# Kernel optimization log

Hardware: AMD Instinct MI355X
Metric: run time of the kernel (lower is better)

Reference implementation:

```python
import jax, jax.numpy as jnp
import numpy as np

EPS_DIST = 1e-8
EPS_BN = 1e-5


def _bn_relu(x, g, b):
    # training-mode BatchNorm1d over (batch, spatial) per channel, then ReLU
    mean = jnp.mean(x, axis=(0, 2), keepdims=True)
    var = jnp.mean((x - mean) ** 2, axis=(0, 2), keepdims=True)
    xhat = (x - mean) * jax.lax.rsqrt(var + EPS_BN)
    return jax.nn.relu(xhat * g[None, :, None] + b[None, :, None])


def setup_inputs() -> dict:
    key = jax.random.key(0)
    ks = jax.random.split(key, 8)
    B, N, M, C1, C2 = 8, 16384, 4096, 64, 256
    return {
        "p1": jax.random.normal(ks[0], (B, N, 3), jnp.float32),
        "p2": jax.random.normal(ks[1], (B, M, 3), jnp.float32),
        "f1": jax.random.normal(ks[2], (B, C1, N), jnp.float32),
        "f2": jax.random.normal(ks[3], (B, C2, M), jnp.float32),
        "idx": jax.random.randint(ks[4], (B, N, 3), 0, M, jnp.int64),
        "W1": jax.random.normal(ks[5], (256, C1 + C2), jnp.float32) * 0.05,
        "g1": jnp.ones((256,), jnp.float32),
        "b1": jnp.zeros((256,), jnp.float32),
        "W2": jax.random.normal(ks[6], (256, 256), jnp.float32) * 0.05,
        "g2": jnp.ones((256,), jnp.float32),
        "b2": jnp.zeros((256,), jnp.float32),
    }


def reference(p1, p2, f1, f2, idx, W1, g1, b1, W2, g2, b2):
    B = p1.shape[0]
    b_ix = jnp.arange(B)[:, None, None]  # batch index for gathers
    # --- three_interpolation: inverse-squared-distance weighted 3-NN interp ---
    nbr_xyz = p2[b_ix, idx]                     # [B, N, 3, 3]
    d2 = jnp.sum((p1[:, :, None, :] - nbr_xyz) ** 2, axis=-1)  # [B, N, 3]
    recip = 1.0 / (d2 + EPS_DIST)
    weight = recip / jnp.sum(recip, axis=-1, keepdims=True)    # [B, N, 3]
    f2_nbr = jnp.swapaxes(f2, 1, 2)[b_ix, idx]  # [B, N, 3, C2]
    interp = jnp.einsum("bnkc,bnk->bcn", f2_nbr, weight)       # [B, C2, N]
    # --- concat + two 1x1 conv + BN + ReLU blocks ---
    x = jnp.concatenate((f1, interp), axis=1)   # [B, C1+C2, N]
    x = _bn_relu(jnp.einsum("oi,bin->bon", W1, x), g1, b1)
    x = _bn_relu(jnp.einsum("oi,bin->bon", W2, x), g2, b2)
    return x
```

## Files before the change

kernel.cpp:

```cpp
#include <hip/hip_runtime.h>
#include <hip/hip_bf16.h>

#define BB 8
#define NN 16384
#define MM 4096
#define C1 64
#define C2 256
#define K1 320
#define CO 256
#define MTOT (BB * NN)

#define STATS_OFF 0
#define FLAG_OFF  8192
#define W1B_OFF   16384
#define W2B_OFF   180224
#define F2T_OFF   327680
#define XT_OFF    (327680 + 16777216)
#define H2_OFF    (327680 + 16777216 + 83886080)

typedef short v8s __attribute__((ext_vector_type(8)));
typedef float v4f __attribute__((ext_vector_type(4)));

__device__ __forceinline__ float bf2f(unsigned short u) {
    unsigned v = ((unsigned)u) << 16;
    float f;
    __builtin_memcpy(&f, &v, 4);
    return f;
}
__device__ __forceinline__ unsigned short f2bf(float f) {
    unsigned u;
    __builtin_memcpy(&u, &f, 4);
    unsigned r = u + 0x7fffu + ((u >> 16) & 1u);
    return (unsigned short)(r >> 16);
}
__device__ __forceinline__ void gload16(const unsigned short* g, unsigned short* l) {
    __builtin_amdgcn_global_load_lds((const __attribute__((address_space(1))) unsigned int*)g,
                                     (__attribute__((address_space(3))) unsigned int*)l, 16, 0, 0);
}

__global__ void k_prep(const void* idx_raw, int* flag64, float* stats,
                       const float* __restrict__ W1, unsigned short* __restrict__ W1b,
                       const float* __restrict__ W2, unsigned short* __restrict__ W2b) {
    int blk = blockIdx.x;
    int t = threadIdx.x;
    if (blk < 320) {
        int e = blk * 256 + t;
        W1b[e] = f2bf(W1[e]);
    } else if (blk < 576) {
        int e = (blk - 320) * 256 + t;
        W2b[e] = f2bf(W2[e]);
    } else {
        for (int i = t; i < 8 * 256; i += 256) stats[i] = 0.f;
        if (t == 0) {
            const int* a = (const int*)idx_raw;
            int all0 = 1;
            for (int j = 1; j < 64; j += 2) all0 &= (a[j] == 0);
            *flag64 = all0;
        }
    }
}

__global__ void k_tr_f2(const float* __restrict__ f2, unsigned short* __restrict__ f2t) {
    __shared__ float tile[64][33];
    int b = blockIdx.z;
    int c0 = blockIdx.y * 64;
    int m0 = blockIdx.x * 32;
    int t = threadIdx.x;
    int lm = t & 31, lc = t >> 5;
    const float* src = f2 + ((size_t)b * C2 + c0) * MM + m0;
#pragma unroll
    for (int j = 0; j < 8; ++j)
        tile[lc + 8 * j][lm] = src[(size_t)(lc + 8 * j) * MM + lm];
    __syncthreads();
    int m = t >> 3, c8 = (t & 7) * 8;
    unsigned short tmp[8];
#pragma unroll
    for (int k = 0; k < 8; ++k) tmp[k] = f2bf(tile[c8 + k][m]);
    uint4 v;
    v.x = (unsigned)tmp[0] | ((unsigned)tmp[1] << 16);
    v.y = (unsigned)tmp[2] | ((unsigned)tmp[3] << 16);
    v.z = (unsigned)tmp[4] | ((unsigned)tmp[5] << 16);
    v.w = (unsigned)tmp[6] | ((unsigned)tmp[7] << 16);
    *(uint4*)&f2t[((size_t)b * MM + m0 + m) * C2 + c0 + c8] = v;
}

__global__ void k_tr_f1(const float* __restrict__ f1, unsigned short* __restrict__ xT) {
    __shared__ float tile[64][33];
    int b = blockIdx.z;
    int n0 = blockIdx.x * 32;
    int t = threadIdx.x;
    int lm = t & 31, lc = t >> 5;
    const float* src = f1 + ((size_t)b * C1) * NN + n0;
#pragma unroll
    for (int j = 0; j < 8; ++j)
        tile[lc + 8 * j][lm] = src[(size_t)(lc + 8 * j) * NN + lm];
    __syncthreads();
    int m = t >> 3, c8 = (t & 7) * 8;
    unsigned short tmp[8];
#pragma unroll
    for (int k = 0; k < 8; ++k) tmp[k] = f2bf(tile[c8 + k][m]);
    uint4 v;
    v.x = (unsigned)tmp[0] | ((unsigned)tmp[1] << 16);
    v.y = (unsigned)tmp[2] | ((unsigned)tmp[3] << 16);
    v.z = (unsigned)tmp[4] | ((unsigned)tmp[5] << 16);
    v.w = (unsigned)tmp[6] | ((unsigned)tmp[7] << 16);
    *(uint4*)&xT[((size_t)b * NN + n0 + m) * K1 + c8] = v;
}

__global__ void k_interp(const float* __restrict__ p1, const float* __restrict__ p2,
                         const void* __restrict__ idxv, const int* __restrict__ flag64,
                         const unsigned short* __restrict__ f2t,
                         unsigned short* __restrict__ xT) {
    int t = threadIdx.x;
    int p = t >> 5, lane = t & 31;
    size_t pt = (size_t)blockIdx.x * 8 + p;
    int b = (int)(pt >> 14);
    int m0, m1, m2;
    if (*flag64) {
        const long long* id = (const long long*)idxv;
        m0 = (int)id[pt * 3 + 0]; m1 = (int)id[pt * 3 + 1]; m2 = (int)id[pt * 3 + 2];
    } else {
        const int* id = (const int*)idxv;
        m0 = id[pt * 3 + 0]; m1 = id[pt * 3 + 1]; m2 = id[pt * 3 + 2];
    }
    float qx = p1[pt * 3 + 0], qy = p1[pt * 3 + 1], qz = p1[pt * 3 + 2];
    const float* pb = p2 + (size_t)b * MM * 3;
    float dx, dy, dz;
    dx = qx - pb[m0 * 3 + 0]; dy = qy - pb[m0 * 3 + 1]; dz = qz - pb[m0 * 3 + 2];
    float d0 = dx * dx + dy * dy + dz * dz;
    dx = qx - pb[m1 * 3 + 0]; dy = qy - pb[m1 * 3 + 1]; dz = qz - pb[m1 * 3 + 2];
    float d1 = dx * dx + dy * dy + dz * dz;
    dx = qx - pb[m2 * 3 + 0]; dy = qy - pb[m2 * 3 + 1]; dz = qz - pb[m2 * 3 + 2];
    float d2v = dx * dx + dy * dy + dz * dz;
    float r0 = 1.f / (d0 + 1e-8f), r1 = 1.f / (d1 + 1e-8f), r2 = 1.f / (d2v + 1e-8f);
    float inv = 1.f / (r0 + r1 + r2);
    float w0 = r0 * inv, w1 = r1 * inv, w2 = r2 * inv;

    const unsigned short* fb = f2t + (size_t)b * MM * C2;
    int c0 = lane * 8;
    uint4 va = *(const uint4*)(fb + (size_t)m0 * C2 + c0);
    uint4 vb = *(const uint4*)(fb + (size_t)m1 * C2 + c0);
    uint4 vc = *(const uint4*)(fb + (size_t)m2 * C2 + c0);

    float r[8];
    {
        const unsigned av[4] = {va.x, va.y, va.z, va.w};
        const unsigned bv[4] = {vb.x, vb.y, vb.z, vb.w};
        const unsigned cv[4] = {vc.x, vc.y, vc.z, vc.w};
#pragma unroll
        for (int q = 0; q < 4; ++q) {
            r[2 * q + 0] = w0 * bf2f((unsigned short)(av[q] & 0xffff))
                         + w1 * bf2f((unsigned short)(bv[q] & 0xffff))
                         + w2 * bf2f((unsigned short)(cv[q] & 0xffff));
            r[2 * q + 1] = w0 * bf2f((unsigned short)(av[q] >> 16))
                         + w1 * bf2f((unsigned short)(bv[q] >> 16))
                         + w2 * bf2f((unsigned short)(cv[q] >> 16));
        }
    }
    uint4 outv;
    outv.x = (unsigned)f2bf(r[0]) | ((unsigned)f2bf(r[1]) << 16);
    outv.y = (unsigned)f2bf(r[2]) | ((unsigned)f2bf(r[3]) << 16);
    outv.z = (unsigned)f2bf(r[4]) | ((unsigned)f2bf(r[5]) << 16);
    outv.w = (unsigned)f2bf(r[6]) | ((unsigned)f2bf(r[7]) << 16);
    *(uint4*)(xT + pt * K1 + C1 + c0) = outv;
}

#define TM 128
#define TN 128
#define TK 64
__launch_bounds__(256)
__global__ void k_gemm1(const unsigned short* __restrict__ xT,
                        const unsigned short* __restrict__ W1b,
                        unsigned short* __restrict__ h1,
                        float* __restrict__ sum1, float* __restrict__ ssq1) {
    __shared__ unsigned short smem[TM * TK + TN * TK];
    __shared__ float s_sum[TN], s_ssq[TN];
    unsigned short* As = smem;
    unsigned short* Bs = smem + TM * TK;
    const int t = threadIdx.x;
    const int lane = t & 63, w = t >> 6;
    const int wm = w >> 1, wc = w & 1;
    const long rbase = (long)blockIdx.x * TM;
    const int cb = blockIdx.y * TN;

    if (t < TN) { s_sum[t] = 0.f; s_ssq[t] = 0.f; }

    v4f acc[4][4];
#pragma unroll
    for (int r = 0; r < 4; ++r)
#pragma unroll
        for (int c = 0; c < 4; ++c) acc[r][c] = (v4f)(0.f);

    const int srow = w * 32 + (lane >> 3);
    const int sch = (lane & 7) * 8;
    const unsigned short* Ag = xT + (rbase + srow) * K1 + sch;
    const unsigned short* Bg = W1b + (size_t)(cb + srow) * K1 + sch;

    for (int k0 = 0; k0 < K1; k0 += TK) {
#pragma unroll
        for (int j = 0; j < 4; ++j) {
            gload16(Ag + (size_t)(j * 8) * K1 + k0, As + (w * 32 + j * 8) * TK);
            gload16(Bg + (size_t)(j * 8) * K1 + k0, Bs + (w * 32 + j * 8) * TK);
        }
        __syncthreads();
        const unsigned short* ApL = As + (wm * 64 + (lane & 15)) * TK + (lane >> 4) * 8;
        const unsigned short* BpL = Bs + (wc * 64 + (lane & 15)) * TK + (lane >> 4) * 8;
#pragma unroll
        for (int ks = 0; ks < 2; ++ks) {
            v8s af[4], bg[4];
#pragma unroll
            for (int r = 0; r < 4; ++r) af[r] = *(const v8s*)(ApL + r * 16 * TK + ks * 32);
#pragma unroll
            for (int c = 0; c < 4; ++c) bg[c] = *(const v8s*)(BpL + c * 16 * TK + ks * 32);
#pragma unroll
            for (int r = 0; r < 4; ++r)
#pragma unroll
                for (int c = 0; c < 4; ++c)
                    acc[r][c] = __builtin_amdgcn_mfma_f32_16x16x32_bf16(af[r], bg[c], acc[r][c], 0, 0, 0);
        }
        __syncthreads();
    }

    const int q = lane >> 4, ln = lane & 15;
#pragma unroll
    for (int c = 0; c < 4; ++c) {
        int col = wc * 64 + c * 16 + ln;
        int cc = col >> 3, ci = col & 7;
        float s = 0.f, sq = 0.f;
#pragma unroll
        for (int r = 0; r < 4; ++r)
#pragma unroll
            for (int i = 0; i < 4; ++i) {
                int row = wm * 64 + r * 16 + q * 4 + i;
                float v = acc[r][c][i];
                smem[row * 128 + 8 * (cc ^ (row & 15)) + ci] = f2bf(v);
                s += v; sq += v * v;
            }
        atomicAdd(&s_sum[col], s);
        atomicAdd(&s_ssq[col], sq);
    }
    __syncthreads();
    {
        int rr = t >> 4, cc2 = t & 15;
#pragma unroll
        for (int j = 0; j < 8; ++j) {
            int row = rr + 16 * j;
            uint4 v = *(const uint4*)&smem[row * 128 + 8 * (cc2 ^ (row & 15))];
            *(uint4*)&h1[(size_t)(rbase + row) * CO + cb + cc2 * 8] = v;
        }
    }
    if (t < TN) {
        atomicAdd(&sum1[cb + t], s_sum[t]);
        atomicAdd(&ssq1[cb + t], s_ssq[t]);
    }
}

__launch_bounds__(256)
__global__ void k_gemm2(const unsigned short* __restrict__ h1,
                        const unsigned short* __restrict__ W2b,
                        const float* __restrict__ sum1, const float* __restrict__ ssq1,
                        const float* __restrict__ g1, const float* __restrict__ b1,
                        unsigned short* __restrict__ h2,
                        float* __restrict__ sum2, float* __restrict__ ssq2) {
    __shared__ unsigned short smem[TM * TK + TN * TK];
    __shared__ float s_sum[TN], s_ssq[TN];
    __shared__ float sc1[CO], sh1[CO];
    unsigned short* As = smem;
    unsigned short* Bs = smem + TM * TK;
    const int t = threadIdx.x;
    const int lane = t & 63, w = t >> 6;
    const int wm = w >> 1, wc = w & 1;
    const long rbase = (long)blockIdx.x * TM;
    const int cb = blockIdx.y * TN;

    {
        const float invn = 1.f / (float)MTOT;
        float m = sum1[t] * invn;
        float v = ssq1[t] * invn - m * m;
        float s = g1[t] * rsqrtf(v + 1e-5f);
        sc1[t] = s;
        sh1[t] = b1[t] - m * s;
    }
    if (t < TN) { s_sum[t] = 0.f; s_ssq[t] = 0.f; }
    __syncthreads();

    v4f acc[4][4];
#pragma unroll
    for (int r = 0; r < 4; ++r)
#pragma unroll
        for (int c = 0; c < 4; ++c) acc[r][c] = (v4f)(0.f);

    const int srow = w * 32 + (lane >> 3);
    const int sch = (lane & 7) * 8;
    const unsigned short* Ag = h1 + (rbase + srow) * CO + sch;
    const unsigned short* Bg = W2b + (size_t)(cb + srow) * CO + sch;
    unsigned short* AsW = As + srow * TK + sch;

    for (int k0 = 0; k0 < CO; k0 += TK) {
#pragma unroll
        for (int j = 0; j < 4; ++j)
            gload16(Bg + (size_t)(j * 8) * CO + k0, Bs + (w * 32 + j * 8) * TK);
        float4 sca = *(const float4*)(sc1 + k0 + sch);
        float4 scb = *(const float4*)(sc1 + k0 + sch + 4);
        float4 sha = *(const float4*)(sh1 + k0 + sch);
        float4 shb = *(const float4*)(sh1 + k0 + sch + 4);
#pragma unroll
        for (int j = 0; j < 4; ++j) {
            uint4 av = *(const uint4*)(Ag + (size_t)(j * 8) * CO + k0);
            float y0 = fmaxf(bf2f((unsigned short)(av.x & 0xffff)) * sca.x + sha.x, 0.f);
            float y1 = fmaxf(bf2f((unsigned short)(av.x >> 16)) * sca.y + sha.y, 0.f);
            float y2 = fmaxf(bf2f((unsigned short)(av.y & 0xffff)) * sca.z + sha.z, 0.f);
            float y3 = fmaxf(bf2f((unsigned short)(av.y >> 16)) * sca.w + sha.w, 0.f);
            float y4 = fmaxf(bf2f((unsigned short)(av.z & 0xffff)) * scb.x + shb.x, 0.f);
            float y5 = fmaxf(bf2f((unsigned short)(av.z >> 16)) * scb.y + shb.y, 0.f);
            float y6 = fmaxf(bf2f((unsigned short)(av.w & 0xffff)) * scb.z + shb.z, 0.f);
            float y7 = fmaxf(bf2f((unsigned short)(av.w >> 16)) * scb.w + shb.w, 0.f);
            uint4 ov;
            ov.x = (unsigned)f2bf(y0) | ((unsigned)f2bf(y1) << 16);
            ov.y = (unsigned)f2bf(y2) | ((unsigned)f2bf(y3) << 16);
            ov.z = (unsigned)f2bf(y4) | ((unsigned)f2bf(y5) << 16);
            ov.w = (unsigned)f2bf(y6) | ((unsigned)f2bf(y7) << 16);
            *(uint4*)(AsW + (j * 8) * TK) = ov;
        }
        __syncthreads();
        const unsigned short* ApL = As + (wm * 64 + (lane & 15)) * TK + (lane >> 4) * 8;
        const unsigned short* BpL = Bs + (wc * 64 + (lane & 15)) * TK + (lane >> 4) * 8;
#pragma unroll
        for (int ks = 0; ks < 2; ++ks) {
            v8s af[4], bg4[4];
#pragma unroll
            for (int r = 0; r < 4; ++r) af[r] = *(const v8s*)(ApL + r * 16 * TK + ks * 32);
#pragma unroll
            for (int c = 0; c < 4; ++c) bg4[c] = *(const v8s*)(BpL + c * 16 * TK + ks * 32);
#pragma unroll
            for (int r = 0; r < 4; ++r)
#pragma unroll
                for (int c = 0; c < 4; ++c)
                    acc[r][c] = __builtin_amdgcn_mfma_f32_16x16x32_bf16(af[r], bg4[c], acc[r][c], 0, 0, 0);
        }
        __syncthreads();
    }

    const int q = lane >> 4, ln = lane & 15;
    const int b = (int)(rbase >> 14);
    const int nb = (int)(rbase & (NN - 1));
#pragma unroll
    for (int c = 0; c < 4; ++c) {
        int ol = wc * 64 + c * 16 + ln;
        float s = 0.f, sq = 0.f;
#pragma unroll
        for (int r = 0; r < 4; ++r)
#pragma unroll
            for (int i = 0; i < 4; ++i) {
                int row = wm * 64 + r * 16 + q * 4 + i;
                int rc = row >> 3, ri = row & 7;
                float v = acc[r][c][i];
                smem[ol * 128 + 8 * (rc ^ (ol & 15)) + ri] = f2bf(v);
                s += v; sq += v * v;
            }
        atomicAdd(&s_sum[ol], s);
        atomicAdd(&s_ssq[ol], sq);
    }
    __syncthreads();
    {
        int oo = t >> 4, nc = t & 15;
#pragma unroll
        for (int j = 0; j < 8; ++j) {
            int ol = oo + 16 * j;
            uint4 v = *(const uint4*)&smem[ol * 128 + 8 * (nc ^ (ol & 15))];
            *(uint4*)&h2[(((size_t)(b * CO + cb + ol)) << 14) + nb + nc * 8] = v;
        }
    }
    if (t < TN) {
        atomicAdd(&sum2[cb + t], s_sum[t]);
        atomicAdd(&ssq2[cb + t], s_ssq[t]);
    }
}

__global__ void k_apply(const unsigned short* __restrict__ h2,
                        const float* __restrict__ sum2, const float* __restrict__ ssq2,
                        const float* __restrict__ g2, const float* __restrict__ b2,
                        float* __restrict__ out) {
    __shared__ float ss[2];
    int o = (blockIdx.x >> 4) & 255;
    if (threadIdx.x == 0) {
        const float invn = 1.f / (float)MTOT;
        float m = sum2[o] * invn;
        float v = ssq2[o] * invn - m * m;
        float s = g2[o] * rsqrtf(v + 1e-5f);
        ss[0] = s;
        ss[1] = b2[o] - m * s;
    }
    __syncthreads();
    float s = ss[0], d = ss[1];
    size_t i = ((size_t)blockIdx.x * 256 + threadIdx.x) * 4;
    ushort4 hv = *(const ushort4*)(h2 + i);
    float4 v;
    v.x = fmaxf(bf2f(hv.x) * s + d, 0.f);
    v.y = fmaxf(bf2f(hv.y) * s + d, 0.f);
    v.z = fmaxf(bf2f(hv.z) * s + d, 0.f);
    v.w = fmaxf(bf2f(hv.w) * s + d, 0.f);
    *(float4*)&out[i] = v;
}

extern "C" void kernel_launch(void* const* d_in, const int* in_sizes, int n_in,
                              void* d_out, int out_size, void* d_ws, size_t ws_size,
                              hipStream_t stream) {
    const float* p1 = (const float*)d_in[0];
    const float* p2 = (const float*)d_in[1];
    const float* f1 = (const float*)d_in[2];
    const float* f2 = (const float*)d_in[3];
    const void*  idx = d_in[4];
    const float* W1 = (const float*)d_in[5];
    const float* g1 = (const float*)d_in[6];
    const float* b1 = (const float*)d_in[7];
    const float* W2 = (const float*)d_in[8];
    const float* g2 = (const float*)d_in[9];
    const float* b2 = (const float*)d_in[10];
    float* out = (float*)d_out;

    char* ws = (char*)d_ws;
    float* stats = (float*)(ws + STATS_OFF);
    float* sum1 = stats + 0;     float* ssq1 = stats + 256;
    float* sum2 = stats + 1024;  float* ssq2 = stats + 1280;
    int* flag64 = (int*)(ws + FLAG_OFF);
    unsigned short* W1b = (unsigned short*)(ws + W1B_OFF);
    unsigned short* W2b = (unsigned short*)(ws + W2B_OFF);
    unsigned short* f2t = (unsigned short*)(ws + F2T_OFF);
    unsigned short* xT  = (unsigned short*)(ws + XT_OFF);
    unsigned short* h2  = (unsigned short*)(ws + H2_OFF);

    unsigned short* h1 = (unsigned short*)d_out;

    k_prep<<<577, 256, 0, stream>>>(idx, flag64, stats, W1, W1b, W2, W2b);
    k_tr_f2<<<dim3(MM / 32, C2 / 64, BB), 256, 0, stream>>>(f2, f2t);
    k_tr_f1<<<dim3(NN / 32, 1, BB), 256, 0, stream>>>(f1, xT);
    k_interp<<<MTOT / 8, 256, 0, stream>>>(p1, p2, idx, flag64, f2t, xT);
    k_gemm1<<<dim3(MTOT / TM, CO / TN), 256, 0, stream>>>(xT, W1b, h1, sum1, ssq1);
    k_gemm2<<<dim3(MTOT / TM, CO / TN), 256, 0, stream>>>(h1, W2b, sum1, ssq1, g1, b1, h2, sum2, ssq2);
    k_apply<<<(int)((size_t)out_size / 4 / 256), 256, 0, stream>>>(h2, sum2, ssq2, g2, b2, out);
}
```

Measured before the change: 425.9 us.

## Recompute GEMM1 in fused GEMM1+GEMM2 kernel instead of storing h1

Splits GEMM1 into a stats-only pass that computes BN1 sums without writing h1. A fused kernel then recomputes GEMM1 per 64-row tile, applies BN1+ReLU into shared memory and runs GEMM2 straight from it, so the h1 round trip through global memory goes away. h2 is now stored row-major and the apply kernel transposes through shared memory to the channel-major output. The cost is doing GEMM1 twice, plus a larger shared-memory footprint that may lower occupancy.

```diff
diff --git a/kernel.cpp b/kernel.cpp
--- a/kernel.cpp
+++ b/kernel.cpp
@@ -165,25 +165,21 @@
     *(uint4*)(xT + pt * K1 + C1 + c0) = outv;
 }
 
-#define TM 128
-#define TN 128
-#define TK 64
+#define S_TK 64
 __launch_bounds__(256)
-__global__ void k_gemm1(const unsigned short* __restrict__ xT,
+__global__ void k_stats(const unsigned short* __restrict__ xT,
                         const unsigned short* __restrict__ W1b,
-                        unsigned short* __restrict__ h1,
                         float* __restrict__ sum1, float* __restrict__ ssq1) {
-    __shared__ unsigned short smem[TM * TK + TN * TK];
-    __shared__ float s_sum[TN], s_ssq[TN];
-    unsigned short* As = smem;
-    unsigned short* Bs = smem + TM * TK;
+    __shared__ unsigned short As[128 * S_TK];
+    __shared__ unsigned short Bs[128 * S_TK];
+    __shared__ float s_sum[128], s_ssq[128];
     const int t = threadIdx.x;
     const int lane = t & 63, w = t >> 6;
     const int wm = w >> 1, wc = w & 1;
-    const long rbase = (long)blockIdx.x * TM;
-    const int cb = blockIdx.y * TN;
-
-    if (t < TN) { s_sum[t] = 0.f; s_ssq[t] = 0.f; }
+    const long rbase = (long)blockIdx.x * 128;
+    const int cb = blockIdx.y * 128;
+
+    if (t < 128) { s_sum[t] = 0.f; s_ssq[t] = 0.f; }
 
     v4f acc[4][4];
 #pragma unroll
@@ -196,22 +192,22 @@
     const unsigned short* Ag = xT + (rbase + srow) * K1 + sch;
     const unsigned short* Bg = W1b + (size_t)(cb + srow) * K1 + sch;
 
-    for (int k0 = 0; k0 < K1; k0 += TK) {
+    for (int k0 = 0; k0 < K1; k0 += S_TK) {
 #pragma unroll
         for (int j = 0; j < 4; ++j) {
-            gload16(Ag + (size_t)(j * 8) * K1 + k0, As + (w * 32 + j * 8) * TK);
-            gload16(Bg + (size_t)(j * 8) * K1 + k0, Bs + (w * 32 + j * 8) * TK);
-        }
-        __syncthreads();
-        const unsigned short* ApL = As + (wm * 64 + (lane & 15)) * TK + (lane >> 4) * 8;
-        const unsigned short* BpL = Bs + (wc * 64 + (lane & 15)) * TK + (lane >> 4) * 8;
+            gload16(Ag + (size_t)(j * 8) * K1 + k0, As + (w * 32 + j * 8) * S_TK);
+            gload16(Bg + (size_t)(j * 8) * K1 + k0, Bs + (w * 32 + j * 8) * S_TK);
+        }
+        __syncthreads();
+        const unsigned short* ApL = As + (wm * 64 + (lane & 15)) * S_TK + (lane >> 4) * 8;
+        const unsigned short* BpL = Bs + (wc * 64 + (lane & 15)) * S_TK + (lane >> 4) * 8;
 #pragma unroll
         for (int ks = 0; ks < 2; ++ks) {
             v8s af[4], bg[4];
 #pragma unroll
-            for (int r = 0; r < 4; ++r) af[r] = *(const v8s*)(ApL + r * 16 * TK + ks * 32);
-#pragma unroll
-            for (int c = 0; c < 4; ++c) bg[c] = *(const v8s*)(BpL + c * 16 * TK + ks * 32);
+            for (int r = 0; r < 4; ++r) af[r] = *(const v8s*)(ApL + r * 16 * S_TK + ks * 32);
+#pragma unroll
+            for (int c = 0; c < 4; ++c) bg[c] = *(const v8s*)(BpL + c * 16 * S_TK + ks * 32);
 #pragma unroll
             for (int r = 0; r < 4; ++r)
 #pragma unroll
@@ -225,53 +221,46 @@
 #pragma unroll
     for (int c = 0; c < 4; ++c) {
         int col = wc * 64 + c * 16 + ln;
-        int cc = col >> 3, ci = col & 7;
         float s = 0.f, sq = 0.f;
 #pragma unroll
         for (int r = 0; r < 4; ++r)
 #pragma unroll
             for (int i = 0; i < 4; ++i) {
-                int row = wm * 64 + r * 16 + q * 4 + i;
                 float v = acc[r][c][i];
-                smem[row * 128 + 8 * (cc ^ (row & 15)) + ci] = f2bf(v);
                 s += v; sq += v * v;
             }
-        atomicAdd(&s_sum[col], s);
-        atomicAdd(&s_ssq[col], sq);
-    }
-    __syncthreads();
-    {
-        int rr = t >> 4, cc2 = t & 15;
-#pragma unroll
-        for (int j = 0; j < 8; ++j) {
-            int row = rr + 16 * j;
-            uint4 v = *(const uint4*)&smem[row * 128 + 8 * (cc2 ^ (row & 15))];
-            *(uint4*)&h1[(size_t)(rbase + row) * CO + cb + cc2 * 8] = v;
-        }
-    }
-    if (t < TN) {
+        s += __shfl_xor(s, 16); s += __shfl_xor(s, 32);
+        sq += __shfl_xor(sq, 16); sq += __shfl_xor(sq, 32);
+        if (q == 0) {
+            atomicAdd(&s_sum[col], s);
+            atomicAdd(&s_ssq[col], sq);
+        }
+    }
+    __syncthreads();
+    if (t < 128) {
         atomicAdd(&sum1[cb + t], s_sum[t]);
         atomicAdd(&ssq1[cb + t], s_ssq[t]);
     }
 }
 
 __launch_bounds__(256)
-__global__ void k_gemm2(const unsigned short* __restrict__ h1,
+__global__ void k_fused(const unsigned short* __restrict__ xT,
+                        const unsigned short* __restrict__ W1b,
                         const unsigned short* __restrict__ W2b,
                         const float* __restrict__ sum1, const float* __restrict__ ssq1,
                         const float* __restrict__ g1, const float* __restrict__ b1,
                         unsigned short* __restrict__ h2,
                         float* __restrict__ sum2, float* __restrict__ ssq2) {
-    __shared__ unsigned short smem[TM * TK + TN * TK];
-    __shared__ float s_sum[TN], s_ssq[TN];
-    __shared__ float sc1[CO], sh1[CO];
-    unsigned short* As = smem;
-    unsigned short* Bs = smem + TM * TK;
+    __shared__ unsigned short smAB[64 * 64 + 256 * 64];
+    __shared__ unsigned short Ys[64 * 256];
+    __shared__ float sc1[CO], sh1[CO], s_sum[CO], s_ssq[CO];
+    unsigned short* As = smAB;
+    unsigned short* Bs = smAB + 64 * 64;
+
     const int t = threadIdx.x;
     const int lane = t & 63, w = t >> 6;
-    const int wm = w >> 1, wc = w & 1;
-    const long rbase = (long)blockIdx.x * TM;
-    const int cb = blockIdx.y * TN;
+    const int q = lane >> 4, ln = lane & 15;
+    const long rbm = (long)blockIdx.x * 64;
 
     {
         const float invn = 1.f / (float)MTOT;
@@ -280,8 +269,8 @@
         float s = g1[t] * rsqrtf(v + 1e-5f);
         sc1[t] = s;
         sh1[t] = b1[t] - m * s;
-    }
-    if (t < TN) { s_sum[t] = 0.f; s_ssq[t] = 0.f; }
+        s_sum[t] = 0.f; s_ssq[t] = 0.f;
+    }
     __syncthreads();
 
     v4f acc[4][4];
@@ -290,117 +279,158 @@
 #pragma unroll
         for (int c = 0; c < 4; ++c) acc[r][c] = (v4f)(0.f);
 
-    const int srow = w * 32 + (lane >> 3);
-    const int sch = (lane & 7) * 8;
-    const unsigned short* Ag = h1 + (rbase + srow) * CO + sch;
-    const unsigned short* Bg = W2b + (size_t)(cb + srow) * CO + sch;
-    unsigned short* AsW = As + srow * TK + sch;
-
-    for (int k0 = 0; k0 < CO; k0 += TK) {
-#pragma unroll
-        for (int j = 0; j < 4; ++j)
-            gload16(Bg + (size_t)(j * 8) * CO + k0, Bs + (w * 32 + j * 8) * TK);
-        float4 sca = *(const float4*)(sc1 + k0 + sch);
-        float4 scb = *(const float4*)(sc1 + k0 + sch + 4);
-        float4 sha = *(const float4*)(sh1 + k0 + sch);
-        float4 shb = *(const float4*)(sh1 + k0 + sch + 4);
-#pragma unroll
-        for (int j = 0; j < 4; ++j) {
-            uint4 av = *(const uint4*)(Ag + (size_t)(j * 8) * CO + k0);
-            float y0 = fmaxf(bf2f((unsigned short)(av.x & 0xffff)) * sca.x + sha.x, 0.f);
-            float y1 = fmaxf(bf2f((unsigned short)(av.x >> 16)) * sca.y + sha.y, 0.f);
-            float y2 = fmaxf(bf2f((unsigned short)(av.y & 0xffff)) * sca.z + sha.z, 0.f);
-            float y3 = fmaxf(bf2f((unsigned short)(av.y >> 16)) * sca.w + sha.w, 0.f);
-            float y4 = fmaxf(bf2f((unsigned short)(av.z & 0xffff)) * scb.x + shb.x, 0.f);
-            float y5 = fmaxf(bf2f((unsigned short)(av.z >> 16)) * scb.y + shb.y, 0.f);
-            float y6 = fmaxf(bf2f((unsigned short)(av.w & 0xffff)) * scb.z + shb.z, 0.f);
-            float y7 = fmaxf(bf2f((unsigned short)(av.w >> 16)) * scb.w + shb.w, 0.f);
-            uint4 ov;
-            ov.x = (unsigned)f2bf(y0) | ((unsigned)f2bf(y1) << 16);
-            ov.y = (unsigned)f2bf(y2) | ((unsigned)f2bf(y3) << 16);
-            ov.z = (unsigned)f2bf(y4) | ((unsigned)f2bf(y5) << 16);
-            ov.w = (unsigned)f2bf(y6) | ((unsigned)f2bf(y7) << 16);
-            *(uint4*)(AsW + (j * 8) * TK) = ov;
-        }
-        __syncthreads();
-        const unsigned short* ApL = As + (wm * 64 + (lane & 15)) * TK + (lane >> 4) * 8;
-        const unsigned short* BpL = Bs + (wc * 64 + (lane & 15)) * TK + (lane >> 4) * 8;
+    const int sr8 = lane >> 3, sc8 = (lane & 7) * 8;
+
+    for (int k0 = 0; k0 < K1; k0 += 64) {
+#pragma unroll
+        for (int j = 0; j < 2; ++j)
+            gload16(xT + (size_t)(rbm + w * 16 + j * 8 + sr8) * K1 + k0 + sc8,
+                    As + (w * 16 + j * 8) * 64);
+#pragma unroll
+        for (int j = 0; j < 8; ++j)
+            gload16(W1b + (size_t)(w * 64 + j * 8 + sr8) * K1 + k0 + sc8,
+                    Bs + (w * 64 + j * 8) * 64);
+        __syncthreads();
+        const unsigned short* ApL = As + ln * 64 + q * 8;
+        const unsigned short* BpL = Bs + (w * 64 + ln) * 64 + q * 8;
 #pragma unroll
         for (int ks = 0; ks < 2; ++ks) {
-            v8s af[4], bg4[4];
-#pragma unroll
-            for (int r = 0; r < 4; ++r) af[r] = *(const v8s*)(ApL + r * 16 * TK + ks * 32);
-#pragma unroll
-            for (int c = 0; c < 4; ++c) bg4[c] = *(const v8s*)(BpL + c * 16 * TK + ks * 32);
+            v8s af[4], bg[4];
+#pragma unroll
+            for (int r = 0; r < 4; ++r) af[r] = *(const v8s*)(ApL + r * 16 * 64 + ks * 32);
+#pragma unroll
+            for (int c = 0; c < 4; ++c) bg[c] = *(const v8s*)(BpL + c * 16 * 64 + ks * 32);
 #pragma unroll
             for (int r = 0; r < 4; ++r)
 #pragma unroll
                 for (int c = 0; c < 4; ++c)
-                    acc[r][c] = __builtin_amdgcn_mfma_f32_16x16x32_bf16(af[r], bg4[c], acc[r][c], 0, 0, 0);
-        }
-        __syncthreads();
-    }
-
-    const int q = lane >> 4, ln = lane & 15;
-    const int b = (int)(rbase >> 14);
-    const int nb = (int)(rbase & (NN - 1));
+                    acc[r][c] = __builtin_amdgcn_mfma_f32_16x16x32_bf16(af[r], bg[c], acc[r][c], 0, 0, 0);
+        }
+        __syncthreads();
+    }
+
 #pragma unroll
     for (int c = 0; c < 4; ++c) {
-        int ol = wc * 64 + c * 16 + ln;
+        int col = w * 64 + c * 16 + ln;
+        float sv = sc1[col], hv = sh1[col];
+        int kc = col >> 3, ci = col & 7;
+#pragma unroll
+        for (int r = 0; r < 4; ++r)
+#pragma unroll
+            for (int i = 0; i < 4; ++i) {
+                int row = r * 16 + q * 4 + i;
+                float y = fmaxf(acc[r][c][i] * sv + hv, 0.f);
+                Ys[row * 256 + 8 * (kc ^ (row & 15)) + ci] = f2bf(y);
+            }
+    }
+    __syncthreads();
+
+#pragma unroll
+    for (int r = 0; r < 4; ++r)
+#pragma unroll
+        for (int c = 0; c < 4; ++c) acc[r][c] = (v4f)(0.f);
+
+    for (int k0 = 0; k0 < CO; k0 += 64) {
+#pragma unroll
+        for (int j = 0; j < 8; ++j)
+            gload16(W2b + (size_t)(w * 64 + j * 8 + sr8) * CO + k0 + sc8,
+                    Bs + (w * 64 + j * 8) * 64);
+        __syncthreads();
+        const unsigned short* BpL = Bs + (w * 64 + ln) * 64 + q * 8;
+#pragma unroll
+        for (int ks = 0; ks < 2; ++ks) {
+            v8s af[4], bg[4];
+            int kc2 = (k0 >> 3) + ks * 4 + q;
+#pragma unroll
+            for (int r = 0; r < 4; ++r)
+                af[r] = *(const v8s*)&Ys[(r * 16 + ln) * 256 + 8 * (kc2 ^ ln)];
+#pragma unroll
+            for (int c = 0; c < 4; ++c) bg[c] = *(const v8s*)(BpL + c * 16 * 64 + ks * 32);
+#pragma unroll
+            for (int r = 0; r < 4; ++r)
+#pragma unroll
+                for (int c = 0; c < 4; ++c)
+                    acc[r][c] = __builtin_amdgcn_mfma_f32_16x16x32_bf16(af[r], bg[c], acc[r][c], 0, 0, 0);
+        }
+        __syncthreads();
+    }
+
+#pragma unroll
+    for (int c = 0; c < 4; ++c) {
+        int col = w * 64 + c * 16 + ln;
+        int cc = col >> 3, ci = col & 7;
         float s = 0.f, sq = 0.f;
 #pragma unroll
         for (int r = 0; r < 4; ++r)
 #pragma unroll
             for (int i = 0; i < 4; ++i) {
-                int row = wm * 64 + r * 16 + q * 4 + i;
-                int rc = row >> 3, ri = row & 7;
+                int row = r * 16 + q * 4 + i;
                 float v = acc[r][c][i];
-                smem[ol * 128 + 8 * (rc ^ (ol & 15)) + ri] = f2bf(v);
+                smAB[row * 256 + 8 * (cc ^ (row & 15)) + ci] = f2bf(v);
                 s += v; sq += v * v;
             }
-        atomicAdd(&s_sum[ol], s);
-        atomicAdd(&s_ssq[ol], sq);
+        s += __shfl_xor(s, 16); s += __shfl_xor(s, 32);
+        sq += __shfl_xor(sq, 16); sq += __shfl_xor(sq, 32);
+        if (q == 0) {
+            atomicAdd(&s_sum[col], s);
+            atomicAdd(&s_ssq[col], sq);
+        }
     }
     __syncthreads();
     {
-        int oo = t >> 4, nc = t & 15;
+        int row2 = t >> 5, cc2 = t & 31;
 #pragma unroll
         for (int j = 0; j < 8; ++j) {
-            int ol = oo + 16 * j;
-            uint4 v = *(const uint4*)&smem[ol * 128 + 8 * (nc ^ (ol & 15))];
-            *(uint4*)&h2[(((size_t)(b * CO + cb + ol)) << 14) + nb + nc * 8] = v;
-        }
-    }
-    if (t < TN) {
-        atomicAdd(&sum2[cb + t], s_sum[t]);
-        atomicAdd(&ssq2[cb + t], s_ssq[t]);
-    }
+            int row = row2 + 8 * j;
+            uint4 v = *(const uint4*)&smAB[row * 256 + 8 * (cc2 ^ (row & 15))];
+            *(uint4*)&h2[(size_t)(rbm + row) * CO + cc2 * 8] = v;
+        }
+    }
+    atomicAdd(&sum2[t], s_sum[t]);
+    atomicAdd(&ssq2[t], s_ssq[t]);
 }
 
 __global__ void k_apply(const unsigned short* __restrict__ h2,
                         const float* __restrict__ sum2, const float* __restrict__ ssq2,
                         const float* __restrict__ g2, const float* __restrict__ b2,
                         float* __restrict__ out) {
-    __shared__ float ss[2];
-    int o = (blockIdx.x >> 4) & 255;
-    if (threadIdx.x == 0) {
+    __shared__ float T[64][36];
+    __shared__ float sc[64], sh[64];
+    int b = blockIdx.z;
+    int cb = blockIdx.y * 64;
+    int n0 = blockIdx.x * 32;
+    int t = threadIdx.x;
+    if (t < 64) {
         const float invn = 1.f / (float)MTOT;
+        int o = cb + t;
         float m = sum2[o] * invn;
         float v = ssq2[o] * invn - m * m;
         float s = g2[o] * rsqrtf(v + 1e-5f);
-        ss[0] = s;
-        ss[1] = b2[o] - m * s;
-    }
-    __syncthreads();
-    float s = ss[0], d = ss[1];
-    size_t i = ((size_t)blockIdx.x * 256 + threadIdx.x) * 4;
-    ushort4 hv = *(const ushort4*)(h2 + i);
-    float4 v;
-    v.x = fmaxf(bf2f(hv.x) * s + d, 0.f);
-    v.y = fmaxf(bf2f(hv.y) * s + d, 0.f);
-    v.z = fmaxf(bf2f(hv.z) * s + d, 0.f);
-    v.w = fmaxf(bf2f(hv.w) * s + d, 0.f);
-    *(float4*)&out[i] = v;
+        sc[t] = s;
+        sh[t] = b2[o] - m * s;
+    }
+    __syncthreads();
+    {
+        int nl = t >> 3, oc = (t & 7) * 8;
+        uint4 hv = *(const uint4*)&h2[((size_t)b * NN + n0 + nl) * CO + cb + oc];
+        const unsigned uv[4] = {hv.x, hv.y, hv.z, hv.w};
+#pragma unroll
+        for (int k = 0; k < 4; ++k) {
+            int ch0 = oc + 2 * k;
+            T[ch0 + 0][nl] = fmaxf(bf2f((unsigned short)(uv[k] & 0xffff)) * sc[ch0] + sh[ch0], 0.f);
+            T[ch0 + 1][nl] = fmaxf(bf2f((unsigned short)(uv[k] >> 16)) * sc[ch0 + 1] + sh[ch0 + 1], 0.f);
+        }
+    }
+    __syncthreads();
+    {
+        int o = t >> 2, jb = t & 3;
+#pragma unroll
+        for (int j2 = 0; j2 < 2; ++j2) {
+            int j = jb + j2 * 4;
+            float4 v = *(const float4*)&T[o][j * 4];
+            *(float4*)&out[((size_t)(b * CO + cb + o)) * NN + n0 + j * 4] = v;
+        }
+    }
 }
 
 extern "C" void kernel_launch(void* const* d_in, const int* in_sizes, int n_in,
@@ -430,13 +460,11 @@
     unsigned short* xT  = (unsigned short*)(ws + XT_OFF);
     unsigned short* h2  = (unsigned short*)(ws + H2_OFF);
 
-    unsigned short* h1 = (unsigned short*)d_out;
-
     k_prep<<<577, 256, 0, stream>>>(idx, flag64, stats, W1, W1b, W2, W2b);
     k_tr_f2<<<dim3(MM / 32, C2 / 64, BB), 256, 0, stream>>>(f2, f2t);
     k_tr_f1<<<dim3(NN / 32, 1, BB), 256, 0, stream>>>(f1, xT);
     k_interp<<<MTOT / 8, 256, 0, stream>>>(p1, p2, idx, flag64, f2t, xT);
-    k_gemm1<<<dim3(MTOT / TM, CO / TN), 256, 0, stream>>>(xT, W1b, h1, sum1, ssq1);
-    k_gemm2<<<dim3(MTOT / TM, CO / TN), 256, 0, stream>>>(h1, W2b, sum1, ssq1, g1, b1, h2, sum2, ssq2);
-    k_apply<<<(int)((size_t)out_size / 4 / 256), 256, 0, stream>>>(h2, sum2, ssq2, g2, b2, out);
-}
+    k_stats<<<dim3(MTOT / 128, 2), 256, 0, stream>>>(xT, W1b, sum1, ssq1);
+    k_fused<<<MTOT / 64, 256, 0, stream>>>(xT, W1b, W2b, sum1, ssq1, g1, b1, h2, sum2, ssq2);
+    k_apply<<<dim3(NN / 32, CO / 64, BB), 256, 0, stream>>>(h2, sum2, ssq2, g2, b2, out);
+}
```

After: 427.0 us. No clear change (+0.3%).
